# Performance work log

Hardware: AMD Instinct MI355X
Metric: run time of the kernel (lower is better)

The kernel has to match this reference:

```python
import jax, jax.numpy as jnp
import numpy as np

NBINS = 100  # hard-coded in torch.histogram(first, 100)


def setup_inputs() -> dict:
    key = jax.random.key(0)
    k1, k2 = jax.random.split(key)
    z = jax.random.normal(k1, (100000, 16), dtype=jnp.float32)
    cluster_layer = jax.random.normal(k2, (16, 16), dtype=jnp.float32)
    return {"z": z, "cluster_layer": cluster_layer}


def _per_feature_hist(combined):
    """Equal-width per-feature histogram (torch.histogram(x, 100) semantics).
    combined: [N+C, F] -> edges [F, NBINS+1], counts [F, NBINS] (float)."""
    lo = combined.min(axis=0)          # [F]
    hi = combined.max(axis=0)          # [F]
    t = jnp.linspace(0.0, 1.0, NBINS + 1, dtype=combined.dtype)  # [NBINS+1]
    edges = lo[:, None] + (hi - lo)[:, None] * t[None, :]        # [F, NBINS+1]
    # bin assignment: left-closed bins, last bin right-closed (np/torch histogram)
    idx = jax.vmap(lambda e, v: jnp.searchsorted(e, v, side="right"),
                   in_axes=(0, 1))(edges, combined) - 1          # [F, N+C]
    idx = jnp.clip(idx, 0, NBINS - 1)
    counts = jax.vmap(lambda i: jnp.zeros((NBINS,), combined.dtype).at[i].add(1.0))(idx)
    return edges, counts


def _mass_dissimilarity(z, cluster_layer):
    N, F = z.shape
    C = cluster_layer.shape[0]
    combined = jax.lax.stop_gradient(jnp.concatenate([z, cluster_layer], axis=0))  # detach()
    edges, counts = _per_feature_hist(combined)          # [F,101], [F,100]

    # searchsorted(bins, .) - 1, per feature (side='left' like torch default)
    sample_bins = jax.vmap(lambda e, v: jnp.searchsorted(e, v, side="left"),
                           in_axes=(0, 1))(edges, z).T - 1              # [N, F]
    cluster_bins = jax.vmap(lambda e, v: jnp.searchsorted(e, v, side="left"),
                            in_axes=(0, 1))(edges, cluster_layer).T - 1  # [C, F]

    mx = jnp.maximum(sample_bins[:, None, :], cluster_bins[None, :, :])  # [N, C, F]
    mn = jnp.minimum(sample_bins[:, None, :], cluster_bins[None, :, :])  # [N, C, F]

    cum = jnp.cumsum(counts, axis=1)                     # [F, NBINS]
    f_idx = jnp.arange(F)                                # broadcasts over [N, C, F]
    is_zero = mn <= 0
    lo_idx = jnp.where(is_zero, 0, mn - 1)
    lo_sum = cum[f_idx, lo_idx]                          # [N, C, F]
    hi_sum = cum[f_idx, jnp.clip(mx, 0, NBINS - 1)]      # [N, C, F]
    sum_counts = jnp.where(is_zero, hi_sum, hi_sum - lo_sum)

    divisor = jnp.asarray(N + C, z.dtype)
    # len(counts)==1 in the original after reshape(1,1,F,NBINS), so no extra divide
    mass = jnp.sqrt(jnp.sum((sum_counts / divisor) ** 2, axis=2))  # [N, C]
    return mass


def reference(z, cluster_layer):
    # get_Q(z, 'mass'): q = 1/(1+mass), row-normalized
    q = 1.0 / (1.0 + _mass_dissimilarity(z, cluster_layer))
    q = q / jnp.sum(q, axis=1, keepdims=True)
    return q
```

## Files before the change

### kernel.cpp

```cpp
#include <hip/hip_runtime.h>
#include <stdint.h>

#define NBINS 100
#define FF 16
#define CC 16
#define MM_BLOCKS 256
#define MM_THREADS 1024
#define H_BLOCKS 256
#define H_THREADS 1024
#define M_THREADS 256


__device__ __forceinline__ unsigned enc_f(float v) {
    unsigned u = __float_as_uint(v);
    return (u & 0x80000000u) ? ~u : (u | 0x80000000u);
}
__device__ __forceinline__ float dec_f(unsigned e) {
    unsigned u = (e & 0x80000000u) ? (e ^ 0x80000000u) : ~e;
    return __uint_as_float(u);
}
__device__ __forceinline__ unsigned shfl_xor_u(unsigned x, int m) {
    return (unsigned)__shfl_xor((int)x, m, 64);
}
__device__ __forceinline__ float edgeval(float lo, float d, int k) {
    float tt = (k == NBINS) ? 1.0f : __fmul_rn((float)k, 0.01f);
    return __fadd_rn(lo, __fmul_rn(d, tt));
}
__device__ __forceinline__ int search_left(float v, float lo, float dd, float scl) {
    int ig = (int)((v - lo) * scl);
    int a = ig - 3;
    a = a < -1 ? -1 : (a > 95 ? 95 : a);
    int g = a;
#pragma unroll
    for (int j = 1; j <= 5; ++j) g += (edgeval(lo, dd, a + j) < v) ? 1 : 0;
    return g;
}
__device__ __forceinline__ int search_right(float v, float lo, float dd, float scl) {
    int ig = (int)((v - lo) * scl);
    int a = ig - 3;
    a = a < -1 ? -1 : (a > 95 ? 95 : a);
    int g = a;
#pragma unroll
    for (int j = 1; j <= 5; ++j) g += (edgeval(lo, dd, a + j) <= v) ? 1 : 0;
    return g;
}
__device__ __forceinline__ float qlook(const float* cumf, int g) {
    int i = g < 0 ? 0 : (g > NBINS - 1 ? NBINS - 1 : g);
    return cumf[i];
}
__device__ __forceinline__ float plook(const float* cumf, int g) {
    int i = g - 1;
    i = i > NBINS - 1 ? NBINS - 1 : i;
    return (g >= 1) ? cumf[i] : 0.0f;
}

__global__ __launch_bounds__(1024) void k_minmax(const float4* __restrict__ z4,
                                                 const float4* __restrict__ cl4,
                                                 int zn4, int total4,
                                                 unsigned* __restrict__ partials,
                                                 unsigned* __restrict__ counts) {
    int t = threadIdx.x;
    int gtid = blockIdx.x * MM_THREADS + t;
    if (gtid < FF * NBINS) counts[gtid] = 0u;

    unsigned mn[4] = {~0u, ~0u, ~0u, ~0u}, mx[4] = {0u, 0u, 0u, 0u};
    int stride = MM_BLOCKS * MM_THREADS;
    for (int i = gtid; i < total4; i += stride) {
        float4 v = (i < zn4) ? z4[i] : cl4[i - zn4];
        unsigned e;
        e = enc_f(v.x); mn[0] = min(mn[0], e); mx[0] = max(mx[0], e);
        e = enc_f(v.y); mn[1] = min(mn[1], e); mx[1] = max(mx[1], e);
        e = enc_f(v.z); mn[2] = min(mn[2], e); mx[2] = max(mx[2], e);
        e = enc_f(v.w); mn[3] = min(mn[3], e); mx[3] = max(mx[3], e);
    }
#pragma unroll
    for (int off = 4; off < 64; off <<= 1) {
#pragma unroll
        for (int c = 0; c < 4; ++c) {
            mn[c] = min(mn[c], shfl_xor_u(mn[c], off));
            mx[c] = max(mx[c], shfl_xor_u(mx[c], off));
        }
    }
    __shared__ unsigned smin[16][16], smax[16][16];
    int wave = t >> 6, lane = t & 63;
    if (lane < 4) {
#pragma unroll
        for (int c = 0; c < 4; ++c) {
            smin[wave][4 * lane + c] = mn[c];
            smax[wave][4 * lane + c] = mx[c];
        }
    }
    __syncthreads();
    if (t < 16) {
        unsigned um = ~0u, ux = 0u;
#pragma unroll
        for (int w = 0; w < 16; ++w) {
            um = min(um, smin[w][t]);
            ux = max(ux, smax[w][t]);
        }
        partials[blockIdx.x * 32 + t] = um;
        partials[blockIdx.x * 32 + 16 + t] = ux;
    }
}

__global__ __launch_bounds__(1024) void k_hist(const float4* __restrict__ z4,
                                               const float4* __restrict__ cl4,
                                               int zn4, int total4,
                                               const unsigned* __restrict__ partials,
                                               unsigned* __restrict__ counts,
                                               float* __restrict__ params) {
    __shared__ unsigned ulo[16], uhi[16];
    __shared__ float slo[16], sd[16], sscl[16];
    __shared__ unsigned sc[FF * NBINS];
    int t = threadIdx.x;
    for (int i = t; i < FF * NBINS; i += H_THREADS) sc[i] = 0u;
    if (t < 16) { ulo[t] = ~0u; uhi[t] = 0u; }
    __syncthreads();
    {
        int f = t & 15, b0 = (t >> 4) * (MM_BLOCKS / 64);
        unsigned um = ~0u, ux = 0u;
#pragma unroll
        for (int b = b0; b < b0 + MM_BLOCKS / 64; ++b) {
            um = min(um, partials[b * 32 + f]);
            ux = max(ux, partials[b * 32 + 16 + f]);
        }
        atomicMin(&ulo[f], um);
        atomicMax(&uhi[f], ux);
    }
    __syncthreads();
    if (t < 16) {
        float lo = dec_f(ulo[t]), hi = dec_f(uhi[t]);
        float d = __fsub_rn(hi, lo);
        slo[t] = lo; sd[t] = d;
        sscl[t] = d > 0.0f ? 100.0f / d : 0.0f;
        if (blockIdx.x == 0) {
            params[t] = lo; params[16 + t] = d; params[32 + t] = sscl[t];
        }
    }
    __syncthreads();

    int gtid = blockIdx.x * H_THREADS + t;
    int stride = H_BLOCKS * H_THREADS;
    int fb = (4 * gtid) & 15;
    float lo_c[4], d_c[4], scl_c[4];
#pragma unroll
    for (int c = 0; c < 4; ++c) {
        int f = (fb + c) & 15;
        lo_c[c] = slo[f]; d_c[c] = sd[f]; scl_c[c] = sscl[f];
    }
    for (int i = gtid; i < total4; i += stride) {
        float4 v4 = (i < zn4) ? z4[i] : cl4[i - zn4];
        float vv[4] = {v4.x, v4.y, v4.z, v4.w};
#pragma unroll
        for (int c = 0; c < 4; ++c) {
            int f = (fb + c) & 15;
            int g = search_right(vv[c], lo_c[c], d_c[c], scl_c[c]);
            g = g < 0 ? 0 : (g > NBINS - 1 ? NBINS - 1 : g);
            atomicAdd(&sc[f * NBINS + g], 1u);
        }
    }
    __syncthreads();
    for (int i = t; i < FF * NBINS; i += H_THREADS) {
        unsigned c = sc[i];
        if (c) atomicAdd(&counts[i], c);
    }
}

__global__ __launch_bounds__(256) void k_main(const float4* __restrict__ z4, int N,
                                              float inv_div,
                                              const unsigned* __restrict__ counts,
                                              const float* __restrict__ params,
                                              const float* __restrict__ cl,
                                              float* __restrict__ out) {
    __shared__ float sparam[48];
    __shared__ float scnt[FF * NBINS];
    __shared__ float scum[FF * NBINS];
    __shared__ float sqp[CC * 32];
    int t = threadIdx.x;
    if (t < 48) sparam[t] = params[t];
    for (int i = t; i < FF * NBINS; i += M_THREADS) scnt[i] = (float)counts[i];
    __syncthreads();
    {
        int f = t >> 4, j = t & 15;
        int b0 = j * 7;
        float loc[7];
        float s = 0.0f;
#pragma unroll
        for (int k = 0; k < 7; ++k) {
            int b = b0 + k;
            float v = (b < NBINS) ? scnt[f * NBINS + b] : 0.0f;
            s += v;
            loc[k] = s;
        }
        float ss = s;
#pragma unroll
        for (int off = 1; off < 16; off <<= 1) {
            float up = __shfl_up(ss, off, 16);
            if (j >= off) ss += up;
        }
        float pre = ss - s;
#pragma unroll
        for (int k = 0; k < 7; ++k) {
            int b = b0 + k;
            if (b < NBINS) scum[f * NBINS + b] = pre + loc[k];
        }
    }
    __syncthreads();
    {
        int c = t & 15, f = t >> 4;
        float v = cl[c * FF + f];
        int g = search_left(v, sparam[f], sparam[16 + f], sparam[32 + f]);
        const float* cumf = &scum[f * NBINS];
        sqp[c * 32 + 2 * f]     = qlook(cumf, g);
        sqp[c * 32 + 2 * f + 1] = plook(cumf, g);
    }
    __syncthreads();

    int n = blockIdx.x * M_THREADS + t;
    if (n >= N) return;

    float v[FF];
    const float4* zr = z4 + (size_t)n * 4;
    float4 a0 = zr[0], a1 = zr[1], a2 = zr[2], a3 = zr[3];
    v[0] = a0.x; v[1] = a0.y; v[2]  = a0.z; v[3]  = a0.w;
    v[4] = a1.x; v[5] = a1.y; v[6]  = a1.z; v[7]  = a1.w;
    v[8] = a2.x; v[9] = a2.y; v[10] = a2.z; v[11] = a2.w;
    v[12] = a3.x; v[13] = a3.y; v[14] = a3.z; v[15] = a3.w;

    float Qs[FF], Ps[FF];
#pragma unroll
    for (int f = 0; f < FF; ++f) {
        int g = search_left(v[f], sparam[f], sparam[16 + f], sparam[32 + f]);
        const float* cumf = &scum[f * NBINS];
        Qs[f] = qlook(cumf, g);
        Ps[f] = plook(cumf, g);
    }

    float q[CC];
    float rowsum = 0.0f;
#pragma unroll
    for (int c = 0; c < CC; ++c) {
        float acc = 0.0f;
        const float4* qprow = (const float4*)&sqp[c * 32];
#pragma unroll
        for (int f2 = 0; f2 < 8; ++f2) {
            float4 qp = qprow[f2];
            float h0 = fmaxf(Qs[2 * f2], qp.x);
            float l0 = fminf(Ps[2 * f2], qp.y);
            float d0 = h0 - l0;
            acc = fmaf(d0, d0, acc);
            float h1 = fmaxf(Qs[2 * f2 + 1], qp.z);
            float l1 = fminf(Ps[2 * f2 + 1], qp.w);
            float d1 = h1 - l1;
            acc = fmaf(d1, d1, acc);
        }
        float mass = sqrtf(acc) * inv_div;
        float qq = 1.0f / (1.0f + mass);
        q[c] = qq;
        rowsum += qq;
    }

    float* op = out + (size_t)n * CC;
    float4 o;
    o.x = q[0] / rowsum;  o.y = q[1] / rowsum;  o.z = q[2] / rowsum;  o.w = q[3] / rowsum;
    ((float4*)op)[0] = o;
    o.x = q[4] / rowsum;  o.y = q[5] / rowsum;  o.z = q[6] / rowsum;  o.w = q[7] / rowsum;
    ((float4*)op)[1] = o;
    o.x = q[8] / rowsum;  o.y = q[9] / rowsum;  o.z = q[10] / rowsum; o.w = q[11] / rowsum;
    ((float4*)op)[2] = o;
    o.x = q[12] / rowsum; o.y = q[13] / rowsum; o.z = q[14] / rowsum; o.w = q[15] / rowsum;
    ((float4*)op)[3] = o;
}

extern "C" void kernel_launch(void* const* d_in, const int* in_sizes, int n_in,
                              void* d_out, int out_size, void* d_ws, size_t ws_size,
                              hipStream_t stream) {
    const float* cl = (const float*)d_in[1];
    float* out = (float*)d_out;
    int N = in_sizes[0] / FF;

    char* ws = (char*)d_ws;
    unsigned* partials = (unsigned*)(ws);
    unsigned* counts   = (unsigned*)(ws + 32768);
    float*    params   = (float*)(ws + 39168);

    const float4* z4  = (const float4*)d_in[0];
    const float4* cl4 = (const float4*)d_in[1];
    int zn4 = N * FF / 4;
    int total4 = (N + CC) * FF / 4;
    float inv_div = 1.0f / (float)(N + CC);

    k_minmax<<<MM_BLOCKS, MM_THREADS, 0, stream>>>(z4, cl4, zn4, total4,
                                                   partials, counts);
    k_hist<<<H_BLOCKS, H_THREADS, 0, stream>>>(z4, cl4, zn4, total4,
                                               partials, counts, params);
    int mblocks = (N + M_THREADS - 1) / M_THREADS;
    k_main<<<mblocks, M_THREADS, 0, stream>>>(z4, N, inv_div, counts, params,
                                              cl, out);
}
```

Baseline: 86.19 us.

## Fuse histogram and main kernels with a device-wide spin barrier

Merges the histogram kernel and the per-row dissimilarity kernel into one 256-block launch of 512 threads. An atomic-counter grid barrier in global memory separates the histogram accumulation from the cumulative-sum and lookup phase. Edge parameters stay in shared memory instead of round-tripping through a global params buffer. This removes one kernel launch and its dependency gap. In exchange it relies on all blocks being co-resident to avoid deadlock, and it uses fewer threads in the histogram loop.

```diff
diff --git a/kernel.cpp b/kernel.cpp
--- a/kernel.cpp
+++ b/kernel.cpp
@@ -4,11 +4,9 @@
 #define NBINS 100
 #define FF 16
 #define CC 16
-#define MM_BLOCKS 256
+#define GRID 256
 #define MM_THREADS 1024
-#define H_BLOCKS 256
-#define H_THREADS 1024
-#define M_THREADS 256
+#define K2_THREADS 512
 
 
 __device__ __forceinline__ unsigned enc_f(float v) {
@@ -58,13 +56,15 @@
                                                  const float4* __restrict__ cl4,
                                                  int zn4, int total4,
                                                  unsigned* __restrict__ partials,
-                                                 unsigned* __restrict__ counts) {
+                                                 unsigned* __restrict__ counts,
+                                                 unsigned* __restrict__ bar) {
     int t = threadIdx.x;
     int gtid = blockIdx.x * MM_THREADS + t;
     if (gtid < FF * NBINS) counts[gtid] = 0u;
+    if (gtid == FF * NBINS) *bar = 0u;
 
     unsigned mn[4] = {~0u, ~0u, ~0u, ~0u}, mx[4] = {0u, 0u, 0u, 0u};
-    int stride = MM_BLOCKS * MM_THREADS;
+    int stride = GRID * MM_THREADS;
     for (int i = gtid; i < total4; i += stride) {
         float4 v = (i < zn4) ? z4[i] : cl4[i - zn4];
         unsigned e;
@@ -103,24 +103,30 @@
     }
 }
 
-__global__ __launch_bounds__(1024) void k_hist(const float4* __restrict__ z4,
-                                               const float4* __restrict__ cl4,
-                                               int zn4, int total4,
-                                               const unsigned* __restrict__ partials,
-                                               unsigned* __restrict__ counts,
-                                               float* __restrict__ params) {
+__global__ __launch_bounds__(512) void k_rest(
+        const float4* __restrict__ z4, const float4* __restrict__ cl4,
+        int zn4, int total4, int N, float inv_div,
+        const unsigned* __restrict__ partials, unsigned* __restrict__ counts,
+        unsigned* __restrict__ bar, const float* __restrict__ cl,
+        float* __restrict__ out)
+{
     __shared__ unsigned ulo[16], uhi[16];
     __shared__ float slo[16], sd[16], sscl[16];
     __shared__ unsigned sc[FF * NBINS];
+    __shared__ float scum[FF * NBINS];
+    __shared__ float sqp[CC * 32];
     int t = threadIdx.x;
-    for (int i = t; i < FF * NBINS; i += H_THREADS) sc[i] = 0u;
+    int gtid = blockIdx.x * K2_THREADS + t;
+    int gsz = GRID * K2_THREADS;
+
+    for (int i = t; i < FF * NBINS; i += K2_THREADS) sc[i] = 0u;
     if (t < 16) { ulo[t] = ~0u; uhi[t] = 0u; }
     __syncthreads();
     {
-        int f = t & 15, b0 = (t >> 4) * (MM_BLOCKS / 64);
+        int f = t & 15, b0 = (t >> 4) * (GRID / 32);
         unsigned um = ~0u, ux = 0u;
 #pragma unroll
-        for (int b = b0; b < b0 + MM_BLOCKS / 64; ++b) {
+        for (int b = b0; b < b0 + GRID / 32; ++b) {
             um = min(um, partials[b * 32 + f]);
             ux = max(ux, partials[b * 32 + 16 + f]);
         }
@@ -133,14 +139,9 @@
         float d = __fsub_rn(hi, lo);
         slo[t] = lo; sd[t] = d;
         sscl[t] = d > 0.0f ? 100.0f / d : 0.0f;
-        if (blockIdx.x == 0) {
-            params[t] = lo; params[16 + t] = d; params[32 + t] = sscl[t];
-        }
-    }
-    __syncthreads();
-
-    int gtid = blockIdx.x * H_THREADS + t;
-    int stride = H_BLOCKS * H_THREADS;
+    }
+    __syncthreads();
+
     int fb = (4 * gtid) & 15;
     float lo_c[4], d_c[4], scl_c[4];
 #pragma unroll
@@ -148,7 +149,7 @@
         int f = (fb + c) & 15;
         lo_c[c] = slo[f]; d_c[c] = sd[f]; scl_c[c] = sscl[f];
     }
-    for (int i = gtid; i < total4; i += stride) {
+    for (int i = gtid; i < total4; i += gsz) {
         float4 v4 = (i < zn4) ? z4[i] : cl4[i - zn4];
         float vv[4] = {v4.x, v4.y, v4.z, v4.w};
 #pragma unroll
@@ -160,27 +161,22 @@
         }
     }
     __syncthreads();
-    for (int i = t; i < FF * NBINS; i += H_THREADS) {
+    for (int i = t; i < FF * NBINS; i += K2_THREADS) {
         unsigned c = sc[i];
         if (c) atomicAdd(&counts[i], c);
     }
-}
-
-__global__ __launch_bounds__(256) void k_main(const float4* __restrict__ z4, int N,
-                                              float inv_div,
-                                              const unsigned* __restrict__ counts,
-                                              const float* __restrict__ params,
-                                              const float* __restrict__ cl,
-                                              float* __restrict__ out) {
-    __shared__ float sparam[48];
-    __shared__ float scnt[FF * NBINS];
-    __shared__ float scum[FF * NBINS];
-    __shared__ float sqp[CC * 32];
-    int t = threadIdx.x;
-    if (t < 48) sparam[t] = params[t];
-    for (int i = t; i < FF * NBINS; i += M_THREADS) scnt[i] = (float)counts[i];
-    __syncthreads();
-    {
+    __syncthreads();
+
+    if (t == 0) {
+        __hip_atomic_fetch_add(bar, 1u, __ATOMIC_RELEASE, __HIP_MEMORY_SCOPE_AGENT);
+        while (__hip_atomic_load(bar, __ATOMIC_ACQUIRE, __HIP_MEMORY_SCOPE_AGENT)
+               < (unsigned)GRID) {
+            __builtin_amdgcn_s_sleep(2);
+        }
+    }
+    __syncthreads();
+
+    if (t < 256) {
         int f = t >> 4, j = t & 15;
         int b0 = j * 7;
         float loc[7];
@@ -188,7 +184,11 @@
 #pragma unroll
         for (int k = 0; k < 7; ++k) {
             int b = b0 + k;
-            float v = (b < NBINS) ? scnt[f * NBINS + b] : 0.0f;
+            float v = 0.0f;
+            if (b < NBINS)
+                v = (float)__hip_atomic_load(&counts[f * NBINS + b],
+                                             __ATOMIC_RELAXED,
+                                             __HIP_MEMORY_SCOPE_AGENT);
             s += v;
             loc[k] = s;
         }
@@ -206,17 +206,17 @@
         }
     }
     __syncthreads();
-    {
+    if (t < CC * FF) {
         int c = t & 15, f = t >> 4;
         float v = cl[c * FF + f];
-        int g = search_left(v, sparam[f], sparam[16 + f], sparam[32 + f]);
+        int g = search_left(v, slo[f], sd[f], sscl[f]);
         const float* cumf = &scum[f * NBINS];
         sqp[c * 32 + 2 * f]     = qlook(cumf, g);
         sqp[c * 32 + 2 * f + 1] = plook(cumf, g);
     }
     __syncthreads();
 
-    int n = blockIdx.x * M_THREADS + t;
+    int n = gtid;
     if (n >= N) return;
 
     float v[FF];
@@ -230,7 +230,7 @@
     float Qs[FF], Ps[FF];
 #pragma unroll
     for (int f = 0; f < FF; ++f) {
-        int g = search_left(v[f], sparam[f], sparam[16 + f], sparam[32 + f]);
+        int g = search_left(v[f], slo[f], sd[f], sscl[f]);
         const float* cumf = &scum[f * NBINS];
         Qs[f] = qlook(cumf, g);
         Ps[f] = plook(cumf, g);
@@ -282,7 +282,7 @@
     char* ws = (char*)d_ws;
     unsigned* partials = (unsigned*)(ws);
     unsigned* counts   = (unsigned*)(ws + 32768);
-    float*    params   = (float*)(ws + 39168);
+    unsigned* bar      = (unsigned*)(ws + 39168);
 
     const float4* z4  = (const float4*)d_in[0];
     const float4* cl4 = (const float4*)d_in[1];
@@ -290,11 +290,8 @@
     int total4 = (N + CC) * FF / 4;
     float inv_div = 1.0f / (float)(N + CC);
 
-    k_minmax<<<MM_BLOCKS, MM_THREADS, 0, stream>>>(z4, cl4, zn4, total4,
-                                                   partials, counts);
-    k_hist<<<H_BLOCKS, H_THREADS, 0, stream>>>(z4, cl4, zn4, total4,
-                                               partials, counts, params);
-    int mblocks = (N + M_THREADS - 1) / M_THREADS;
-    k_main<<<mblocks, M_THREADS, 0, stream>>>(z4, N, inv_div, counts, params,
-                                              cl, out);
-}
+    k_minmax<<<GRID, MM_THREADS, 0, stream>>>(z4, cl4, zn4, total4,
+                                              partials, counts, bar);
+    k_rest<<<GRID, K2_THREADS, 0, stream>>>(z4, cl4, zn4, total4, N, inv_div,
+                                            partials, counts, bar, cl, out);
+}
```

New measurement: 94.78 us. 10.0% more time.
